# Optimization experiments

Hardware: AMD Instinct MI355X
Metric: run time of the kernel (lower is better)

Reference implementation:

```python
import jax, jax.numpy as jnp
import numpy as np

N = 100000      # nodes
E = 1600000     # directed edges (before self-loops)
DIN = 128       # input feature dim
HID = 32        # per-head hidden dim
HEADS = 4
D1 = HID * HEADS  # 128, concat width
NG = 64         # graphs in batch
NEG_SLOPE = 0.2 # PyG GATConv leaky_relu slope


def setup_inputs() -> dict:
    key = jax.random.key(0)
    ks = jax.random.split(key, 16)
    s = 0.05
    x = jax.random.normal(ks[0], (N, DIN), dtype=jnp.float32)
    edge_index = jax.random.randint(ks[1], (2, E), 0, N, dtype=jnp.int32)
    batch = jnp.sort(jax.random.randint(ks[2], (N,), 0, NG, dtype=jnp.int32))
    # GATConv 1: in=DIN, out=HID, heads=HEADS, concat=True
    W1 = jax.random.normal(ks[3], (D1, DIN), dtype=jnp.float32) * s
    a1s = jax.random.normal(ks[4], (HEADS, HID), dtype=jnp.float32) * s
    a1d = jax.random.normal(ks[5], (HEADS, HID), dtype=jnp.float32) * s
    b1 = jnp.zeros((D1,), jnp.float32)
    # GATConv 2: in=D1, out=HID, heads=HEADS, concat=True
    W2 = jax.random.normal(ks[6], (D1, D1), dtype=jnp.float32) * s
    a2s = jax.random.normal(ks[7], (HEADS, HID), dtype=jnp.float32) * s
    a2d = jax.random.normal(ks[8], (HEADS, HID), dtype=jnp.float32) * s
    b2 = jnp.zeros((D1,), jnp.float32)
    # GATConv 3: in=D1, out=HID, heads=HEADS, concat=False (mean over heads)
    W3 = jax.random.normal(ks[9], (D1, D1), dtype=jnp.float32) * s
    a3s = jax.random.normal(ks[10], (HEADS, HID), dtype=jnp.float32) * s
    a3d = jax.random.normal(ks[11], (HEADS, HID), dtype=jnp.float32) * s
    b3 = jnp.zeros((HID,), jnp.float32)
    lin_w = jax.random.normal(ks[12], (1, HID), dtype=jnp.float32) * s
    lin_b = jnp.zeros((1,), jnp.float32)
    return {"x": x, "edge_index": edge_index, "batch": batch,
            "W1": W1, "a1s": a1s, "a1d": a1d, "b1": b1,
            "W2": W2, "a2s": a2s, "a2d": a2d, "b2": b2,
            "W3": W3, "a3s": a3s, "a3d": a3d, "b3": b3,
            "lin_w": lin_w, "lin_b": lin_b}


def _gat_conv(x, ei, W, att_src, att_dst, bias, concat):
    """PyG GATConv (no edge features, self-loops already in ei)."""
    n = x.shape[0]
    h = (x @ W.T).reshape(n, HEADS, HID)          # [N, H, C]
    src, dst = ei[0], ei[1]
    a_src = jnp.einsum('nhc,hc->nh', h, att_src)  # [N, H]
    a_dst = jnp.einsum('nhc,hc->nh', h, att_dst)
    e = jax.nn.leaky_relu(a_src[src] + a_dst[dst], NEG_SLOPE)  # [Etot, H]
    # segment softmax over incoming edges of each dst node
    e_max = jax.ops.segment_max(e, dst, num_segments=n)
    ex = jnp.exp(e - e_max[dst])
    denom = jax.ops.segment_sum(ex, dst, num_segments=n)
    alpha = ex / denom[dst]                        # [Etot, H]
    out = jax.ops.segment_sum(h[src] * alpha[:, :, None], dst, num_segments=n)
    if concat:
        out = out.reshape(n, HEADS * HID)
    else:
        out = out.mean(axis=1)
    return out + bias


def reference(x, edge_index, batch, W1, a1s, a1d, b1, W2, a2s, a2d, b2,
              W3, a3s, a3d, b3, lin_w, lin_b):
    loops = jnp.arange(N, dtype=edge_index.dtype)
    ei = jnp.concatenate([edge_index, jnp.stack([loops, loops])], axis=1)
    h = jax.nn.elu(_gat_conv(x, ei, W1, a1s, a1d, b1, True))
    h = jax.nn.elu(_gat_conv(h, ei, W2, a2s, a2d, b2, True))
    h = jax.nn.elu(_gat_conv(h, ei, W3, a3s, a3d, b3, False))
    h = h @ lin_w.T + lin_b                        # [N, 1]
    counts = jax.ops.segment_sum(jnp.ones((N,), h.dtype), batch, num_segments=NG)
    pooled = jax.ops.segment_sum(h, batch, num_segments=NG) / counts[:, None]
    return pooled.squeeze()                        # [NG]
```

## Files before the change

kernel.cpp:

```cpp
#include <hip/hip_runtime.h>
#include <hip/hip_fp16.h>
#include <math.h>

#define D1 128
#define NEG 0.2f
#define NODE_SHIFT 9
#define BIN_NODES 512
#define MAXBIN 256

typedef short v8s __attribute__((ext_vector_type(8)));
typedef float v4f __attribute__((ext_vector_type(4)));

__device__ __forceinline__ float lrelu(float v){ return v > 0.f ? v : NEG * v; }
__device__ __forceinline__ float elu_f(float v){ return v > 0.f ? v : __expf(v) - 1.f; }

__device__ __forceinline__ unsigned short bf16s(float f){
    unsigned u = __float_as_uint(f);
    return (unsigned short)((u + 0x7fffu + ((u >> 16) & 1u)) >> 16);
}
__device__ __forceinline__ float bf2f(unsigned short s){
    return __uint_as_float(((unsigned)s) << 16);
}
__device__ __forceinline__ unsigned f2h2(float a, float b){
    return ((unsigned)__half_as_ushort(__float2half_rn(b)) << 16) |
           (unsigned)__half_as_ushort(__float2half_rn(a));
}
__device__ __forceinline__ float2 h2f2(unsigned u){
    float lo = __half2float(__ushort_as_half((unsigned short)(u & 0xffffu)));
    float hi = __half2float(__ushort_as_half((unsigned short)(u >> 16)));
    return make_float2(lo, hi);
}
__device__ __forceinline__ void split8(const float* f, v8s& hi, v8s& lo){
    #pragma unroll
    for (int i = 0; i < 8; i++){
        unsigned short h = bf16s(f[i]);
        ((short*)&hi)[i] = (short)h;
        ((short*)&lo)[i] = (short)bf16s(f[i] - bf2f(h));
    }
}


__global__ __launch_bounds__(256) void kb_hist(const int* __restrict__ ei,
                                               int* __restrict__ binCnt,
                                               int n_edges, int etot, int nbin){
    __shared__ int h[MAXBIN];
    for (int i = threadIdx.x; i < nbin; i += 256) h[i] = 0;
    __syncthreads();
    int stride = gridDim.x * 256;
    for (int e = blockIdx.x * 256 + threadIdx.x; e < etot; e += stride){
        int dst = (e < n_edges) ? ei[n_edges + e] : (e - n_edges);
        atomicAdd(&h[dst >> NODE_SHIFT], 1);
    }
    __syncthreads();
    for (int i = threadIdx.x; i < nbin; i += 256)
        if (h[i]) atomicAdd(&binCnt[i], h[i]);
}

__global__ void kb_scan(const int* __restrict__ binCnt, int* __restrict__ binStart,
                        int* __restrict__ binCursor, int nbin,
                        int* __restrict__ rowptr, int n_nodes, int etot){
    if (threadIdx.x == 0){
        int run = 0;
        for (int b = 0; b < nbin; b++){
            binStart[b] = run; binCursor[b] = run; run += binCnt[b];
        }
        binStart[nbin] = run;
        rowptr[n_nodes] = etot;
    }
}

__global__ __launch_bounds__(256) void kb_scatter(const int* __restrict__ ei,
                                                  int* __restrict__ binCursor,
                                                  unsigned* __restrict__ staged,
                                                  int n_edges, int etot, int nbin){
    __shared__ int cnt[MAXBIN];
    __shared__ int base[MAXBIN];
    int e0 = blockIdx.x * 4096;
    for (int i = threadIdx.x; i < nbin; i += 256) cnt[i] = 0;
    __syncthreads();
    #pragma unroll 4
    for (int r = 0; r < 16; r++){
        int e = e0 + r * 256 + threadIdx.x;
        if (e < etot){
            int dst = (e < n_edges) ? ei[n_edges + e] : (e - n_edges);
            atomicAdd(&cnt[dst >> NODE_SHIFT], 1);
        }
    }
    __syncthreads();
    for (int i = threadIdx.x; i < nbin; i += 256){
        base[i] = cnt[i] ? atomicAdd(&binCursor[i], cnt[i]) : 0;
        cnt[i] = 0;
    }
    __syncthreads();
    #pragma unroll 4
    for (int r = 0; r < 16; r++){
        int e = e0 + r * 256 + threadIdx.x;
        if (e < etot){
            int src, dst;
            if (e < n_edges){ src = ei[e]; dst = ei[n_edges + e]; }
            else            { src = dst = e - n_edges; }
            int b = dst >> NODE_SHIFT;
            int p = base[b] + atomicAdd(&cnt[b], 1);
            staged[p] = ((unsigned)(dst & (BIN_NODES - 1)) << 17) | (unsigned)src;
        }
    }
}

__global__ __launch_bounds__(512) void kb_final(const unsigned* __restrict__ staged,
                                                const int* __restrict__ binStart,
                                                int* __restrict__ rowptr,
                                                int* __restrict__ eidx, int n_nodes){
    __shared__ int deg[BIN_NODES];
    __shared__ int cur[BIN_NODES];
    int b = blockIdx.x;
    int nbase = b << NODE_SHIFT;
    int s0 = binStart[b], s1 = binStart[b + 1];
    deg[threadIdx.x] = 0;
    __syncthreads();
    for (int i = s0 + threadIdx.x; i < s1; i += 512)
        atomicAdd(&deg[staged[i] >> 17], 1);
    __syncthreads();
    int v = deg[threadIdx.x];
    cur[threadIdx.x] = v;
    __syncthreads();
    for (int off = 1; off < BIN_NODES; off <<= 1){
        int t = (threadIdx.x >= off) ? cur[threadIdx.x - off] : 0;
        __syncthreads();
        cur[threadIdx.x] += t;
        __syncthreads();
    }
    int excl = cur[threadIdx.x] - v;
    int node = nbase + threadIdx.x;
    if (node < n_nodes) rowptr[node] = s0 + excl;
    cur[threadIdx.x] = s0 + excl;
    __syncthreads();
    for (int i = s0 + threadIdx.x; i < s1; i += 512){
        unsigned pr = staged[i];
        int p = atomicAdd(&cur[pr >> 17], 1);
        eidx[p] = (int)(pr & 0x1FFFFu);
    }
}


__global__ void k_prepw(const float* __restrict__ W1, const float* __restrict__ W2,
                        const float* __restrict__ W3, unsigned short* __restrict__ Bp){
    int t = blockIdx.x * 256 + threadIdx.x;
    if (t >= 49152) return;
    int w = t >> 14;
    int r = t & 16383;
    int k = r >> 7, j = r & 127;
    const float* W = (w == 0) ? W1 : (w == 1) ? W2 : W3;
    float val = W[j * 128 + k];
    unsigned short hi = bf16s(val);
    unsigned short lo = bf16s(val - bf2f(hi));
    int idx = (k >> 3) * 1024 + j * 8 + (k & 7);
    Bp[w * 32768 + idx] = hi;
    Bp[w * 32768 + 16384 + idx] = lo;
}


template<int FP32SRC>
__global__ __launch_bounds__(256, 4) void k_mgemm(
        const float* __restrict__ Xf,
        const unsigned short* __restrict__ Xhi, const unsigned short* __restrict__ Xlo,
        const unsigned short* __restrict__ Bp,
        const float* __restrict__ aw_s, const float* __restrict__ aw_d,
        unsigned short* __restrict__ Hh,
        float* __restrict__ asrc, float* __restrict__ adst, int n_rows){
    __shared__ unsigned short Bs[16384];
    int lane = threadIdx.x & 63;
    int wv   = threadIdx.x >> 6;
    int li = lane & 15, quad = lane >> 4;
    int r0 = blockIdx.x * 128 + wv * 32;

    int row0 = r0 + li;
    int row1 = r0 + 16 + li;
    int rc0 = row0 < n_rows ? row0 : 0;
    int rc1 = row1 < n_rows ? row1 : 0;

    v4f acc[2][8];
    #pragma unroll
    for (int m = 0; m < 2; m++)
        #pragma unroll
        for (int t = 0; t < 8; t++)
            acc[m][t] = (v4f){0.f, 0.f, 0.f, 0.f};

    #pragma unroll
    for (int g = 0; g < 2; g++){
        if (g) __syncthreads();
        #pragma unroll
        for (int i = 0; i < 4; i++){
            int idx = threadIdx.x + i * 256;
            ((float4*)Bs)[idx]          = ((const float4*)(Bp + g * 8192))[idx];
            ((float4*)(Bs + 8192))[idx] = ((const float4*)(Bp + 16384 + g * 8192))[idx];
        }
        __syncthreads();
        #pragma unroll
        for (int ks2 = 0; ks2 < 2; ks2++){
            int ks = g * 2 + ks2;
            int koff = ks * 32 + quad * 8;
            v8s ah0, al0, ah1, al1;
            if (FP32SRC){
                float f0[8], f1[8];
                *(float4*)&f0[0] = *(const float4*)(Xf + (size_t)rc0 * 128 + koff);
                *(float4*)&f0[4] = *(const float4*)(Xf + (size_t)rc0 * 128 + koff + 4);
                *(float4*)&f1[0] = *(const float4*)(Xf + (size_t)rc1 * 128 + koff);
                *(float4*)&f1[4] = *(const float4*)(Xf + (size_t)rc1 * 128 + koff + 4);
                split8(f0, ah0, al0);
                split8(f1, ah1, al1);
            } else {
                ah0 = *(const v8s*)(Xhi + (size_t)rc0 * 128 + koff);
                al0 = *(const v8s*)(Xlo + (size_t)rc0 * 128 + koff);
                ah1 = *(const v8s*)(Xhi + (size_t)rc1 * 128 + koff);
                al1 = *(const v8s*)(Xlo + (size_t)rc1 * 128 + koff);
            }
            #pragma unroll
            for (int t = 0; t < 8; t++){
                int bo = ks2 * 4096 + quad * 1024 + (t * 16 + li) * 8;
                v8s bh = *(const v8s*)(Bs + bo);
                v8s bl = *(const v8s*)(Bs + 8192 + bo);
                acc[0][t] = __builtin_amdgcn_mfma_f32_16x16x32_bf16(ah0, bh, acc[0][t], 0, 0, 0);
                acc[0][t] = __builtin_amdgcn_mfma_f32_16x16x32_bf16(ah0, bl, acc[0][t], 0, 0, 0);
                acc[0][t] = __builtin_amdgcn_mfma_f32_16x16x32_bf16(al0, bh, acc[0][t], 0, 0, 0);
                acc[1][t] = __builtin_amdgcn_mfma_f32_16x16x32_bf16(ah1, bh, acc[1][t], 0, 0, 0);
                acc[1][t] = __builtin_amdgcn_mfma_f32_16x16x32_bf16(ah1, bl, acc[1][t], 0, 0, 0);
                acc[1][t] = __builtin_amdgcn_mfma_f32_16x16x32_bf16(al1, bh, acc[1][t], 0, 0, 0);
            }
        }
    }

    #pragma unroll
    for (int m = 0; m < 2; m++){
        #pragma unroll
        for (int t = 0; t < 8; t++){
            #pragma unroll
            for (int r = 0; r < 4; r++){
                float v  = acc[m][t][r];
                float vo = __shfl_xor(v, 1);
                if (!(li & 1)){
                    int row = r0 + m * 16 + quad * 4 + r;
                    if (row < n_rows)
                        *(unsigned*)(Hh + (size_t)row * 128 + t * 16 + li) = f2h2(v, vo);
                }
            }
        }
    }

    float as8[8], ad8[8];
    #pragma unroll
    for (int t = 0; t < 8; t++){
        as8[t] = aw_s[t * 16 + li];
        ad8[t] = aw_d[t * 16 + li];
    }
    #pragma unroll
    for (int m = 0; m < 2; m++){
        #pragma unroll
        for (int r = 0; r < 4; r++){
            float sp[4], dp[4];
            #pragma unroll
            for (int h = 0; h < 4; h++){
                sp[h] = acc[m][2*h][r] * as8[2*h] + acc[m][2*h+1][r] * as8[2*h+1];
                dp[h] = acc[m][2*h][r] * ad8[2*h] + acc[m][2*h+1][r] * ad8[2*h+1];
            }
            #pragma unroll
            for (int off = 1; off < 16; off <<= 1){
                #pragma unroll
                for (int h = 0; h < 4; h++){
                    sp[h] += __shfl_xor(sp[h], off);
                    dp[h] += __shfl_xor(dp[h], off);
                }
            }
            if (li == 0){
                int row = r0 + m * 16 + quad * 4 + r;
                if (row < n_rows){
                    ((float4*)asrc)[row] = make_float4(sp[0], sp[1], sp[2], sp[3]);
                    ((float4*)adst)[row] = make_float4(dp[0], dp[1], dp[2], dp[3]);
                }
            }
        }
    }
}


template<int MEAN>
__global__ __launch_bounds__(256) void k_aggr(
        const unsigned* __restrict__ Hh,
        const float* __restrict__ asrc, const float* __restrict__ adst,
        const int* __restrict__ rowptr, const int* __restrict__ eidx,
        const float* __restrict__ bias,
        unsigned short* __restrict__ Oh, unsigned short* __restrict__ Ol,
        float* __restrict__ Of, int n_nodes){
    int lane = threadIdx.x & 63;
    int wid  = threadIdx.x >> 6;
    int n = blockIdx.x * 4 + wid;
    if (n >= n_nodes) return;
    int row0 = rowptr[n];
    int deg  = rowptr[n + 1] - row0;
    const int* ep = eidx + row0;
    unsigned hd = (unsigned)(lane >> 4);
    unsigned ul = (unsigned)lane;
    float4 ad = ((const float4*)adst)[n];
    float adh = hd == 0 ? ad.x : hd == 1 ? ad.y : hd == 2 ? ad.z : ad.w;
    unsigned wh = (ul >> 3) & 3;
    float adw = wh == 0 ? ad.x : wh == 1 ? ad.y : wh == 2 ? ad.z : ad.w;
    int wsrc = (int)(hd * 8);

    float accx = 0.f, accy = 0.f, den = 0.f;
    int i = 0;
    for (; i + 8 <= deg; i += 8){
        unsigned s[8];
        #pragma unroll
        for (int j = 0; j < 8; j++) s[j] = (unsigned)ep[i + j];
        float aW = asrc[s[ul & 7] * 4u + wh];
        float w = __expf(lrelu(aW + adw));
        unsigned hw[8];
        #pragma unroll
        for (int j = 0; j < 8; j++) hw[j] = Hh[s[j] * 64u + ul];
        #pragma unroll
        for (int j = 0; j < 8; j++){
            float wj = __shfl(w, wsrc + j);
            float2 hv = h2f2(hw[j]);
            den  += wj;
            accx += wj * hv.x;
            accy += wj * hv.y;
        }
    }
    for (; i < deg; i++){
        unsigned s = (unsigned)ep[i];
        float w = __expf(lrelu(asrc[s * 4u + hd] + adh));
        float2 hv = h2f2(Hh[s * 64u + ul]);
        den  += w;
        accx += w * hv.x;
        accy += w * hv.y;
    }
    float rdh = 1.f / den;
    accx *= rdh; accy *= rdh;

    int c = lane * 2;
    if (!MEAN){
        float ox = elu_f(accx + bias[c]);
        float oy = elu_f(accy + bias[c + 1]);
        unsigned short hx = bf16s(ox), hy = bf16s(oy);
        unsigned short lx = bf16s(ox - bf2f(hx)), ly = bf16s(oy - bf2f(hy));
        *(ushort2*)(Oh + (size_t)n * 128 + c) = make_ushort2(hx, hy);
        *(ushort2*)(Ol + (size_t)n * 128 + c) = make_ushort2(lx, ly);
    } else {
        float sx = accx, sy = accy;
        sx += __shfl_xor(sx, 16); sy += __shfl_xor(sy, 16);
        sx += __shfl_xor(sx, 32); sy += __shfl_xor(sy, 32);
        if (lane < 16){
            int cc = lane * 2;
            float ox = elu_f(sx * 0.25f + bias[cc]);
            float oy = elu_f(sy * 0.25f + bias[cc + 1]);
            *(float2*)(Of + (size_t)n * 32 + cc) = make_float2(ox, oy);
        }
    }
}


__global__ void k_readout(const float* __restrict__ H3, const int* __restrict__ batch,
                          const float* __restrict__ lw, const float* __restrict__ lb,
                          float* __restrict__ pool, float* __restrict__ cnt, int n_nodes){
    __shared__ float pl[64];
    __shared__ float cl[64];
    if (threadIdx.x < 64){ pl[threadIdx.x] = 0.f; cl[threadIdx.x] = 0.f; }
    __syncthreads();
    int n = blockIdx.x * 256 + threadIdx.x;
    if (n < n_nodes){
        const float4* hp = (const float4*)(H3 + (size_t)n * 32);
        const float4* wp = (const float4*)lw;
        float y = 0.f;
        #pragma unroll
        for (int i = 0; i < 8; i++){
            float4 h4 = hp[i], w4 = wp[i];
            y += h4.x * w4.x + h4.y * w4.y + h4.z * w4.z + h4.w * w4.w;
        }
        y += lb[0];
        int b = batch[n];
        atomicAdd(&pl[b], y);
        atomicAdd(&cl[b], 1.f);
    }
    __syncthreads();
    if (threadIdx.x < 64 && cl[threadIdx.x] != 0.f){
        atomicAdd(&pool[threadIdx.x], pl[threadIdx.x]);
        atomicAdd(&cnt[threadIdx.x], cl[threadIdx.x]);
    }
}

__global__ void k_final(const float* __restrict__ pool, const float* __restrict__ cnt,
                        float* __restrict__ out){
    int g = threadIdx.x;
    if (g < 64) out[g] = (cnt[g] > 0.f) ? pool[g] / cnt[g] : 0.f;
}


extern "C" void kernel_launch(void* const* d_in, const int* in_sizes, int n_in,
                              void* d_out, int out_size, void* d_ws, size_t ws_size,
                              hipStream_t stream){
    const float* x   = (const float*)d_in[0];
    const int*   ei  = (const int*)  d_in[1];
    const int*   bat = (const int*)  d_in[2];
    const float* W1  = (const float*)d_in[3];
    const float* a1s = (const float*)d_in[4];
    const float* a1d = (const float*)d_in[5];
    const float* b1  = (const float*)d_in[6];
    const float* W2  = (const float*)d_in[7];
    const float* a2s = (const float*)d_in[8];
    const float* a2d = (const float*)d_in[9];
    const float* b2  = (const float*)d_in[10];
    const float* W3  = (const float*)d_in[11];
    const float* a3s = (const float*)d_in[12];
    const float* a3d = (const float*)d_in[13];
    const float* b3  = (const float*)d_in[14];
    const float* lw  = (const float*)d_in[15];
    const float* lb  = (const float*)d_in[16];
    (void)n_in; (void)out_size; (void)ws_size;

    const int n_nodes = in_sizes[0] / D1;
    const int n_edges = in_sizes[1] / 2;
    const int etot    = n_edges + n_nodes;
    const int nbin    = (n_nodes + BIN_NODES - 1) >> NODE_SHIFT;

    char* p = (char*)d_ws;
    size_t off = 0;
    auto alloc = [&](size_t bytes) -> char* {
        char* r = p + off;
        off = (off + bytes + 511) & ~(size_t)511;
        return r;
    };
    unsigned short* Hh   = (unsigned short*)alloc((size_t)n_nodes * 128 * 2);
    unsigned short* Xhi  = (unsigned short*)alloc((size_t)n_nodes * 128 * 2);
    unsigned short* Xlo  = (unsigned short*)alloc((size_t)n_nodes * 128 * 2);
    float*          asrc = (float*)alloc((size_t)n_nodes * 4 * 4);
    float*          adst = (float*)alloc((size_t)n_nodes * 4 * 4);
    unsigned short* Bp   = (unsigned short*)alloc(3 * 32768 * 2);
    int*      rowptr  = (int*)alloc((size_t)(n_nodes + 1) * 4);
    int*      eidx    = (int*)alloc((size_t)etot * 4);
    unsigned* staged  = (unsigned*)alloc((size_t)etot * 4);
    int*      binCnt  = (int*)alloc(MAXBIN * 4);
    int*      binStart= (int*)alloc((MAXBIN + 1) * 4);
    int*      binCur  = (int*)alloc(MAXBIN * 4);
    float*    pool    = (float*)alloc(64 * 4);
    float*    cnt     = (float*)alloc(64 * 4);
    float*    h3      = (float*)Xhi;

    hipMemsetAsync(binCnt, 0, MAXBIN * 4, stream);
    hipMemsetAsync(pool, 0, 64 * 4, stream);
    hipMemsetAsync(cnt, 0, 64 * 4, stream);

    k_prepw<<<192, 256, 0, stream>>>(W1, W2, W3, Bp);

    int cb = (etot + 4095) / 4096;
    kb_hist<<<cb, 256, 0, stream>>>(ei, binCnt, n_edges, etot, nbin);
    kb_scan<<<1, 64, 0, stream>>>(binCnt, binStart, binCur, nbin, rowptr, n_nodes, etot);
    kb_scatter<<<cb, 256, 0, stream>>>(ei, binCur, staged, n_edges, etot, nbin);
    kb_final<<<nbin, 512, 0, stream>>>(staged, binStart, rowptr, eidx, n_nodes);

    int mb = (n_nodes + 127) / 128;
    int rb = (n_nodes + 3) / 4;

    k_mgemm<1><<<mb, 256, 0, stream>>>(x, nullptr, nullptr, Bp,
                                       a1s, a1d, Hh, asrc, adst, n_nodes);
    k_aggr<0><<<rb, 256, 0, stream>>>((const unsigned*)Hh, asrc, adst, rowptr, eidx,
                                      b1, Xhi, Xlo, nullptr, n_nodes);
    k_mgemm<0><<<mb, 256, 0, stream>>>(nullptr, Xhi, Xlo, Bp + 32768,
                                       a2s, a2d, Hh, asrc, adst, n_nodes);
    k_aggr<0><<<rb, 256, 0, stream>>>((const unsigned*)Hh, asrc, adst, rowptr, eidx,
                                      b2, Xhi, Xlo, nullptr, n_nodes);
    k_mgemm<0><<<mb, 256, 0, stream>>>(nullptr, Xhi, Xlo, Bp + 65536,
                                       a3s, a3d, Hh, asrc, adst, n_nodes);
    k_aggr<1><<<rb, 256, 0, stream>>>((const unsigned*)Hh, asrc, adst, rowptr, eidx,
                                      b3, nullptr, nullptr, h3, n_nodes);

    int ob = (n_nodes + 255) / 256;
    k_readout<<<ob, 256, 0, stream>>>(h3, bat, lw, lb, pool, cnt, n_nodes);
    k_final<<<1, 64, 0, stream>>>(pool, cnt, (float*)d_out);
}
```

Before: 545.7 us.

## Replace split-bf16 triple MFMA GEMM with single fp16 MFMA and fp16 activations

The GEMM kernel drops the hi/lo bf16 error-compensated scheme, which issued three MFMAs per tile, and uses one fp16 MFMA per tile with fp16 weights and activations. Aggregation now writes a single fp16 activation buffer instead of hi and lo bf16 buffers. This cuts MFMA work, the weight LDS footprint, and the activation read and write traffic. The whole weight matrix is now loaded into LDS once, with A operands preloaded before it. The cost is lower precision (fp16 mantissa only), with a risk of accuracy drift or overflow in the intermediates.

```diff
diff --git a/kernel.cpp b/kernel.cpp
--- a/kernel.cpp
+++ b/kernel.cpp
@@ -8,19 +8,12 @@
 #define BIN_NODES 512
 #define MAXBIN 256
 
-typedef short v8s __attribute__((ext_vector_type(8)));
+typedef _Float16 v8h __attribute__((ext_vector_type(8)));
 typedef float v4f __attribute__((ext_vector_type(4)));
 
 __device__ __forceinline__ float lrelu(float v){ return v > 0.f ? v : NEG * v; }
 __device__ __forceinline__ float elu_f(float v){ return v > 0.f ? v : __expf(v) - 1.f; }
 
-__device__ __forceinline__ unsigned short bf16s(float f){
-    unsigned u = __float_as_uint(f);
-    return (unsigned short)((u + 0x7fffu + ((u >> 16) & 1u)) >> 16);
-}
-__device__ __forceinline__ float bf2f(unsigned short s){
-    return __uint_as_float(((unsigned)s) << 16);
-}
 __device__ __forceinline__ unsigned f2h2(float a, float b){
     return ((unsigned)__half_as_ushort(__float2half_rn(b)) << 16) |
            (unsigned)__half_as_ushort(__float2half_rn(a));
@@ -29,14 +22,6 @@
     float lo = __half2float(__ushort_as_half((unsigned short)(u & 0xffffu)));
     float hi = __half2float(__ushort_as_half((unsigned short)(u >> 16)));
     return make_float2(lo, hi);
-}
-__device__ __forceinline__ void split8(const float* f, v8s& hi, v8s& lo){
-    #pragma unroll
-    for (int i = 0; i < 8; i++){
-        unsigned short h = bf16s(f[i]);
-        ((short*)&hi)[i] = (short)h;
-        ((short*)&lo)[i] = (short)bf16s(f[i] - bf2f(h));
-    }
 }
 
 
@@ -151,18 +136,14 @@
     int k = r >> 7, j = r & 127;
     const float* W = (w == 0) ? W1 : (w == 1) ? W2 : W3;
     float val = W[j * 128 + k];
-    unsigned short hi = bf16s(val);
-    unsigned short lo = bf16s(val - bf2f(hi));
     int idx = (k >> 3) * 1024 + j * 8 + (k & 7);
-    Bp[w * 32768 + idx] = hi;
-    Bp[w * 32768 + 16384 + idx] = lo;
+    Bp[w * 16384 + idx] = __half_as_ushort(__float2half_rn(val));
 }
 
 
 template<int FP32SRC>
 __global__ __launch_bounds__(256, 4) void k_mgemm(
-        const float* __restrict__ Xf,
-        const unsigned short* __restrict__ Xhi, const unsigned short* __restrict__ Xlo,
+        const float* __restrict__ Xf, const unsigned short* __restrict__ Xh,
         const unsigned short* __restrict__ Bp,
         const float* __restrict__ aw_s, const float* __restrict__ aw_d,
         unsigned short* __restrict__ Hh,
@@ -178,6 +159,34 @@
     int rc0 = row0 < n_rows ? row0 : 0;
     int rc1 = row1 < n_rows ? row1 : 0;
 
+    v8h a0[4], a1[4];
+    #pragma unroll
+    for (int ks = 0; ks < 4; ks++){
+        int koff = ks * 32 + quad * 8;
+        if (FP32SRC){
+            float f0[8], f1[8];
+            *(float4*)&f0[0] = *(const float4*)(Xf + (size_t)rc0 * 128 + koff);
+            *(float4*)&f0[4] = *(const float4*)(Xf + (size_t)rc0 * 128 + koff + 4);
+            *(float4*)&f1[0] = *(const float4*)(Xf + (size_t)rc1 * 128 + koff);
+            *(float4*)&f1[4] = *(const float4*)(Xf + (size_t)rc1 * 128 + koff + 4);
+            #pragma unroll
+            for (int i = 0; i < 8; i++){
+                a0[ks][i] = (_Float16)f0[i];
+                a1[ks][i] = (_Float16)f1[i];
+            }
+        } else {
+            a0[ks] = *(const v8h*)(Xh + (size_t)rc0 * 128 + koff);
+            a1[ks] = *(const v8h*)(Xh + (size_t)rc1 * 128 + koff);
+        }
+    }
+
+    #pragma unroll
+    for (int i = 0; i < 8; i++){
+        int idx = threadIdx.x + i * 256;
+        ((float4*)Bs)[idx] = ((const float4*)Bp)[idx];
+    }
+    __syncthreads();
+
     v4f acc[2][8];
     #pragma unroll
     for (int m = 0; m < 2; m++)
@@ -186,46 +195,13 @@
             acc[m][t] = (v4f){0.f, 0.f, 0.f, 0.f};
 
     #pragma unroll
-    for (int g = 0; g < 2; g++){
-        if (g) __syncthreads();
-        #pragma unroll
-        for (int i = 0; i < 4; i++){
-            int idx = threadIdx.x + i * 256;
-            ((float4*)Bs)[idx]          = ((const float4*)(Bp + g * 8192))[idx];
-            ((float4*)(Bs + 8192))[idx] = ((const float4*)(Bp + 16384 + g * 8192))[idx];
-        }
-        __syncthreads();
-        #pragma unroll
-        for (int ks2 = 0; ks2 < 2; ks2++){
-            int ks = g * 2 + ks2;
-            int koff = ks * 32 + quad * 8;
-            v8s ah0, al0, ah1, al1;
-            if (FP32SRC){
-                float f0[8], f1[8];
-                *(float4*)&f0[0] = *(const float4*)(Xf + (size_t)rc0 * 128 + koff);
-                *(float4*)&f0[4] = *(const float4*)(Xf + (size_t)rc0 * 128 + koff + 4);
-                *(float4*)&f1[0] = *(const float4*)(Xf + (size_t)rc1 * 128 + koff);
-                *(float4*)&f1[4] = *(const float4*)(Xf + (size_t)rc1 * 128 + koff + 4);
-                split8(f0, ah0, al0);
-                split8(f1, ah1, al1);
-            } else {
-                ah0 = *(const v8s*)(Xhi + (size_t)rc0 * 128 + koff);
-                al0 = *(const v8s*)(Xlo + (size_t)rc0 * 128 + koff);
-                ah1 = *(const v8s*)(Xhi + (size_t)rc1 * 128 + koff);
-                al1 = *(const v8s*)(Xlo + (size_t)rc1 * 128 + koff);
-            }
-            #pragma unroll
-            for (int t = 0; t < 8; t++){
-                int bo = ks2 * 4096 + quad * 1024 + (t * 16 + li) * 8;
-                v8s bh = *(const v8s*)(Bs + bo);
-                v8s bl = *(const v8s*)(Bs + 8192 + bo);
-                acc[0][t] = __builtin_amdgcn_mfma_f32_16x16x32_bf16(ah0, bh, acc[0][t], 0, 0, 0);
-                acc[0][t] = __builtin_amdgcn_mfma_f32_16x16x32_bf16(ah0, bl, acc[0][t], 0, 0, 0);
-                acc[0][t] = __builtin_amdgcn_mfma_f32_16x16x32_bf16(al0, bh, acc[0][t], 0, 0, 0);
-                acc[1][t] = __builtin_amdgcn_mfma_f32_16x16x32_bf16(ah1, bh, acc[1][t], 0, 0, 0);
-                acc[1][t] = __builtin_amdgcn_mfma_f32_16x16x32_bf16(ah1, bl, acc[1][t], 0, 0, 0);
-                acc[1][t] = __builtin_amdgcn_mfma_f32_16x16x32_bf16(al1, bh, acc[1][t], 0, 0, 0);
-            }
+    for (int ks = 0; ks < 4; ks++){
+        #pragma unroll
+        for (int t = 0; t < 8; t++){
+            int bo = (ks * 4 + quad) * 1024 + (t * 16 + li) * 8;
+            v8h b = *(const v8h*)(Bs + bo);
+            acc[0][t] = __builtin_amdgcn_mfma_f32_16x16x32_f16(a0[ks], b, acc[0][t], 0, 0, 0);
+            acc[1][t] = __builtin_amdgcn_mfma_f32_16x16x32_f16(a1[ks], b, acc[1][t], 0, 0, 0);
         }
     }
 
@@ -288,8 +264,7 @@
         const float* __restrict__ asrc, const float* __restrict__ adst,
         const int* __restrict__ rowptr, const int* __restrict__ eidx,
         const float* __restrict__ bias,
-        unsigned short* __restrict__ Oh, unsigned short* __restrict__ Ol,
-        float* __restrict__ Of, int n_nodes){
+        unsigned short* __restrict__ O, float* __restrict__ Of, int n_nodes){
     int lane = threadIdx.x & 63;
     int wid  = threadIdx.x >> 6;
     int n = blockIdx.x * 4 + wid;
@@ -340,10 +315,7 @@
     if (!MEAN){
         float ox = elu_f(accx + bias[c]);
         float oy = elu_f(accy + bias[c + 1]);
-        unsigned short hx = bf16s(ox), hy = bf16s(oy);
-        unsigned short lx = bf16s(ox - bf2f(hx)), ly = bf16s(oy - bf2f(hy));
-        *(ushort2*)(Oh + (size_t)n * 128 + c) = make_ushort2(hx, hy);
-        *(ushort2*)(Ol + (size_t)n * 128 + c) = make_ushort2(lx, ly);
+        *(unsigned*)(O + (size_t)n * 128 + c) = f2h2(ox, oy);
     } else {
         float sx = accx, sy = accy;
         sx += __shfl_xor(sx, 16); sy += __shfl_xor(sy, 16);
@@ -429,11 +401,10 @@
         return r;
     };
     unsigned short* Hh   = (unsigned short*)alloc((size_t)n_nodes * 128 * 2);
-    unsigned short* Xhi  = (unsigned short*)alloc((size_t)n_nodes * 128 * 2);
-    unsigned short* Xlo  = (unsigned short*)alloc((size_t)n_nodes * 128 * 2);
+    unsigned short* Xh   = (unsigned short*)alloc((size_t)n_nodes * 128 * 2);
     float*          asrc = (float*)alloc((size_t)n_nodes * 4 * 4);
     float*          adst = (float*)alloc((size_t)n_nodes * 4 * 4);
-    unsigned short* Bp   = (unsigned short*)alloc(3 * 32768 * 2);
+    unsigned short* Bp   = (unsigned short*)alloc(3 * 16384 * 2);
     int*      rowptr  = (int*)alloc((size_t)(n_nodes + 1) * 4);
     int*      eidx    = (int*)alloc((size_t)etot * 4);
     unsigned* staged  = (unsigned*)alloc((size_t)etot * 4);
@@ -442,7 +413,7 @@
     int*      binCur  = (int*)alloc(MAXBIN * 4);
     float*    pool    = (float*)alloc(64 * 4);
     float*    cnt     = (float*)alloc(64 * 4);
-    float*    h3      = (float*)Xhi;
+    float*    h3      = (float*)Xh;
 
     hipMemsetAsync(binCnt, 0, MAXBIN * 4, stream);
     hipMemsetAsync(pool, 0, 64 * 4, stream);
@@ -459,18 +430,18 @@
     int mb = (n_nodes + 127) / 128;
     int rb = (n_nodes + 3) / 4;
 
-    k_mgemm<1><<<mb, 256, 0, stream>>>(x, nullptr, nullptr, Bp,
+    k_mgemm<1><<<mb, 256, 0, stream>>>(x, nullptr, Bp,
                                        a1s, a1d, Hh, asrc, adst, n_nodes);
     k_aggr<0><<<rb, 256, 0, stream>>>((const unsigned*)Hh, asrc, adst, rowptr, eidx,
-                                      b1, Xhi, Xlo, nullptr, n_nodes);
-    k_mgemm<0><<<mb, 256, 0, stream>>>(nullptr, Xhi, Xlo, Bp + 32768,
+                                      b1, Xh, nullptr, n_nodes);
+    k_mgemm<0><<<mb, 256, 0, stream>>>(nullptr, Xh, Bp + 16384,
                                        a2s, a2d, Hh, asrc, adst, n_nodes);
     k_aggr<0><<<rb, 256, 0, stream>>>((const unsigned*)Hh, asrc, adst, rowptr, eidx,
-                                      b2, Xhi, Xlo, nullptr, n_nodes);
-    k_mgemm<0><<<mb, 256, 0, stream>>>(nullptr, Xhi, Xlo, Bp + 65536,
+                                      b2, Xh, nullptr, n_nodes);
+    k_mgemm<0><<<mb, 256, 0, stream>>>(nullptr, Xh, Bp + 32768,
                                        a3s, a3d, Hh, asrc, adst, n_nodes);
     k_aggr<1><<<rb, 256, 0, stream>>>((const unsigned*)Hh, asrc, adst, rowptr, eidx,
-                                      b3, nullptr, nullptr, h3, n_nodes);
+                                      b3, nullptr, h3, n_nodes);
 
     int ob = (n_nodes + 255) / 256;
     k_readout<<<ob, 256, 0, stream>>>(h3, bat, lw, lb, pool, cnt, n_nodes);
```

New measurement: 522.6 us. 4.2% less time.
